# Kernel tuning notes

Measured on AMD Instinct MI355X. Metric: run time of the kernel, lower is better.

## Reference

```python
import jax, jax.numpy as jnp
import numpy as np

TEMPERATURE = 1.0
EPS = 1e-8
BATCH = 4_194_304
NUM_WEEKS = 262_144


def setup_inputs() -> dict:
    key = jax.random.key(0)
    k1, k2, k3 = jax.random.split(key, 3)
    scores = jax.random.normal(k1, (BATCH,), dtype=jnp.float32)
    labels = jax.random.normal(k2, (BATCH,), dtype=jnp.float32)
    week_indices = jnp.sort(
        jax.random.randint(k3, (BATCH,), 0, NUM_WEEKS, dtype=jnp.int32)
    )
    return {
        "scores": scores,
        "labels": labels,
        "week_indices": week_indices,
        "num_weeks": NUM_WEEKS,
    }


def _segment_softmax(x, seg, num_segments):
    # numerically stable softmax within each segment (week)
    m = jax.ops.segment_max(x, seg, num_segments=num_segments)
    e = jnp.exp(x - m[seg])
    s = jax.ops.segment_sum(e, seg, num_segments=num_segments)
    return e / s[seg]


def reference(scores, labels, week_indices, num_weeks):
    t = jnp.float32(TEMPERATURE)
    p_true = _segment_softmax(labels / t, week_indices, num_weeks)
    p_pred = _segment_softmax(scores / t, week_indices, num_weeks)
    # per-week cross-entropy: -sum p_true * log(p_pred + eps)
    per_item = p_true * jnp.log(p_pred + EPS)
    per_week = jax.ops.segment_sum(per_item, week_indices, num_segments=num_weeks)
    counts = jax.ops.segment_sum(
        jnp.ones_like(scores), week_indices, num_segments=num_weeks
    )
    valid = counts >= 2.0  # weeks with <2 items are skipped
    n_valid = jnp.sum(valid.astype(jnp.float32))
    total = -jnp.sum(jnp.where(valid, per_week, 0.0))
    return jnp.where(n_valid > 0, total / jnp.maximum(n_valid, 1.0), 0.0)
```

## Files before the change

kernel.cpp:

```cpp
#include <hip/hip_runtime.h>
#include <math.h>


#define K 16
#define TPB 256
#define CHUNK (K * TPB)
#define SLOTS 768

__device__ __forceinline__ void lds_flush(float* lel, float* les, float* ltl,
                                          int* lcnt, int s, float a, float b,
                                          float t, int c) {
    atomicAdd(&lel[s], a);
    atomicAdd(&les[s], b);
    atomicAdd(&ltl[s], t);
    atomicAdd(&lcnt[s], c);
}

__global__ __launch_bounds__(TPB) void main_pass(
        const float* __restrict__ scores, const float* __restrict__ labels,
        const int* __restrict__ widx,
        int* __restrict__ rec_week, float* __restrict__ rec_el,
        float* __restrict__ rec_es, float* __restrict__ rec_tl,
        int* __restrict__ rec_cnt,
        float* __restrict__ part_loss, int* __restrict__ part_nv) {
    __shared__ float lel[SLOTS], les[SLOTS], ltl[SLOTS];
    __shared__ int lcnt[SLOTS];
    const int tid = threadIdx.x;
    for (int s = tid; s < SLOTS; s += TPB) {
        lel[s] = 0.f; les[s] = 0.f; ltl[s] = 0.f; lcnt[s] = 0;
    }
    const int base = blockIdx.x * CHUNK;
    const int w0 = widx[base];
    const int wl = widx[base + CHUNK - 1];
    __syncthreads();

    const int t0 = base + tid * K;
    const int4   wA = *reinterpret_cast<const int4*>(widx + t0);
    const int4   wB = *reinterpret_cast<const int4*>(widx + t0 + 4);
    const int4   wC = *reinterpret_cast<const int4*>(widx + t0 + 8);
    const int4   wD = *reinterpret_cast<const int4*>(widx + t0 + 12);
    const float4 lA = *reinterpret_cast<const float4*>(labels + t0);
    const float4 lB = *reinterpret_cast<const float4*>(labels + t0 + 4);
    const float4 lC = *reinterpret_cast<const float4*>(labels + t0 + 8);
    const float4 lD = *reinterpret_cast<const float4*>(labels + t0 + 12);
    const float4 sA = *reinterpret_cast<const float4*>(scores + t0);
    const float4 sB = *reinterpret_cast<const float4*>(scores + t0 + 4);
    const float4 sC = *reinterpret_cast<const float4*>(scores + t0 + 8);
    const float4 sD = *reinterpret_cast<const float4*>(scores + t0 + 12);

    float loss = 0.f; int nv = 0;
    int cw; float ra, rb, rt; int rc;
    bool head_saved = false;
    int hs = 0; float ha = 0.f, hb = 0.f, ht = 0.f; int hc = 0;

    {
        const float el = __expf(lA.x), es = __expf(sA.x);
        cw = wA.x; ra = el; rb = es; rt = el * sA.x; rc = 1;
    }
#define ITEM(wv, lv, sv)                                                       \
    {                                                                          \
        const float el = __expf(lv), es = __expf(sv);                          \
        if ((wv) == cw) { ra += el; rb += es; rt += el * (sv); ++rc; }         \
        else {                                                                 \
            if (!head_saved) {                                                 \
                hs = cw - w0; ha = ra; hb = rb; ht = rt; hc = rc;              \
                head_saved = true;                                             \
            } else if (rc >= 2) {                                              \
                loss += rt / ra - __logf(rb); ++nv;  \
            }                                                                  \
            cw = (wv); ra = el; rb = es; rt = el * (sv); rc = 1;               \
        }                                                                      \
    }
    ITEM(wA.y, lA.y, sA.y) ITEM(wA.z, lA.z, sA.z) ITEM(wA.w, lA.w, sA.w)
    ITEM(wB.x, lB.x, sB.x) ITEM(wB.y, lB.y, sB.y) ITEM(wB.z, lB.z, sB.z) ITEM(wB.w, lB.w, sB.w)
    ITEM(wC.x, lC.x, sC.x) ITEM(wC.y, lC.y, sC.y) ITEM(wC.z, lC.z, sC.z) ITEM(wC.w, lC.w, sC.w)
    ITEM(wD.x, lD.x, sD.x) ITEM(wD.y, lD.y, sD.y) ITEM(wD.z, lD.z, sD.z) ITEM(wD.w, lD.w, sD.w)
#undef ITEM

    if (head_saved) lds_flush(lel, les, ltl, lcnt, hs, ha, hb, ht, hc);
    lds_flush(lel, les, ltl, lcnt, cw - w0, ra, rb, rt, rc);
    __syncthreads();

    const int span = wl - w0;
    for (int s = 1 + tid; s < span; s += TPB) {
        const int c = lcnt[s];
        if (c >= 2) { loss += ltl[s] / lel[s] - __logf(les[s]); ++nv; }
    }
    #pragma unroll
    for (int off = 32; off; off >>= 1) {
        loss += __shfl_down(loss, off);
        nv   += __shfl_down(nv, off);
    }
    __shared__ float ra4[4];
    __shared__ int   rn4[4];
    const int lane = tid & 63, wv4 = tid >> 6;
    if (lane == 0) { ra4[wv4] = loss; rn4[wv4] = nv; }
    __syncthreads();
    if (tid == 0) {
        part_loss[blockIdx.x] = ra4[0] + ra4[1] + ra4[2] + ra4[3];
        part_nv[blockIdx.x]   = rn4[0] + rn4[1] + rn4[2] + rn4[3];
        const int b2 = blockIdx.x * 2;
        rec_week[b2] = w0;
        rec_el[b2] = lel[0]; rec_es[b2] = les[0];
        rec_tl[b2] = ltl[0]; rec_cnt[b2] = lcnt[0];
        rec_week[b2 + 1] = wl;
        if (span > 0) {
            rec_el[b2 + 1] = lel[span]; rec_es[b2 + 1] = les[span];
            rec_tl[b2 + 1] = ltl[span]; rec_cnt[b2 + 1] = lcnt[span];
        } else {
            rec_el[b2 + 1] = 0.f; rec_es[b2 + 1] = 0.f;
            rec_tl[b2 + 1] = 0.f; rec_cnt[b2 + 1] = 0;
        }
    }
}

__global__ __launch_bounds__(1024) void finalize(
        const int* __restrict__ rec_week, const float* __restrict__ rec_el,
        const float* __restrict__ rec_es, const float* __restrict__ rec_tl,
        const int* __restrict__ rec_cnt,
        const float* __restrict__ part_loss, const int* __restrict__ part_nv,
        int nrec, int nb, float* __restrict__ out) {
    const int tid = threadIdx.x;
    float loss = 0.f; int nv = 0;
    for (int j = tid; j < nrec; j += 1024) {
        const int w = rec_week[j];
        if (j > 0 && rec_week[j - 1] == w) continue;
        float a = rec_el[j], b = rec_es[j], t = rec_tl[j];
        int c = rec_cnt[j];
        int k = j + 1;
        while (k < nrec && rec_week[k] == w) {
            a += rec_el[k]; b += rec_es[k]; t += rec_tl[k]; c += rec_cnt[k]; ++k;
        }
        if (c >= 2) { loss += t / a - __logf(b); ++nv; }
    }
    for (int j = tid; j < nb; j += 1024) { loss += part_loss[j]; nv += part_nv[j]; }
    #pragma unroll
    for (int off = 32; off; off >>= 1) {
        loss += __shfl_down(loss, off);
        nv   += __shfl_down(nv, off);
    }
    __shared__ float ra[16];
    __shared__ int   rn[16];
    const int lane = tid & 63, wv = tid >> 6;
    if (lane == 0) { ra[wv] = loss; rn[wv] = nv; }
    __syncthreads();
    if (tid == 0) {
        float tl = 0.f; int tn = 0;
        for (int k = 0; k < 16; ++k) { tl += ra[k]; tn += rn[k]; }
        out[0] = (tn > 0) ? (-tl / (float)tn) : 0.f;
    }
}

extern "C" void kernel_launch(void* const* d_in, const int* in_sizes, int n_in,
                              void* d_out, int out_size, void* d_ws, size_t ws_size,
                              hipStream_t stream) {
    const float* scores = (const float*)d_in[0];
    const float* labels = (const float*)d_in[1];
    const int*   widx   = (const int*)d_in[2];
    const int n  = in_sizes[0];
    const int nb = n / CHUNK;
    const int nrec = nb * 2;

    char* ws = (char*)d_ws;
    size_t off = 0;
    int*   rec_week = (int*)  (ws + off); off += (size_t)nrec * 4;
    float* rec_el   = (float*)(ws + off); off += (size_t)nrec * 4;
    float* rec_es   = (float*)(ws + off); off += (size_t)nrec * 4;
    float* rec_tl   = (float*)(ws + off); off += (size_t)nrec * 4;
    int*   rec_cnt  = (int*)  (ws + off); off += (size_t)nrec * 4;
    float* part_loss= (float*)(ws + off); off += (size_t)nb * 4;
    int*   part_nv  = (int*)  (ws + off);

    float* out = (float*)d_out;

    main_pass<<<nb, TPB, 0, stream>>>(scores, labels, widx,
                                      rec_week, rec_el, rec_es, rec_tl, rec_cnt,
                                      part_loss, part_nv);
    finalize<<<1, 1024, 0, stream>>>(rec_week, rec_el, rec_es, rec_tl, rec_cnt,
                                     part_loss, part_nv, nrec, nb, out);
}
```

Before: 23.22 us.

## Stage inputs through swizzled LDS with coalesced loads in two halves

Each thread no longer loads 16 contiguous elements straight from global memory. The block now loads each half of its chunk with coalesced float4 loads into swizzled shared-memory staging buffers, then each thread reads 8 contiguous elements from LDS. This aims to improve global load coalescing, since the old per-thread 64-byte strided loads were poorly coalesced. In exchange it adds extra barriers, about 24KB more LDS (which may lower occupancy), twice as many boundary flushes per thread, and shorter runs per thread, so there are more LDS atomics.

```diff
diff --git a/kernel.cpp b/kernel.cpp
--- a/kernel.cpp
+++ b/kernel.cpp
@@ -2,10 +2,13 @@
 #include <math.h>
 
 
-#define K 16
 #define TPB 256
-#define CHUNK (K * TPB)
+#define CHUNK 4096
+#define HALF 2048
+#define HF4 512
 #define SLOTS 768
+
+__device__ __forceinline__ int swz(int s) { return s ^ ((s >> 3) & 7); }
 
 __device__ __forceinline__ void lds_flush(float* lel, float* les, float* ltl,
                                           int* lcnt, int s, float a, float b,
@@ -23,6 +26,9 @@
         float* __restrict__ rec_es, float* __restrict__ rec_tl,
         int* __restrict__ rec_cnt,
         float* __restrict__ part_loss, int* __restrict__ part_nv) {
+    __shared__ int4   stg_w[HF4];
+    __shared__ float4 stg_l[HF4];
+    __shared__ float4 stg_s[HF4];
     __shared__ float lel[SLOTS], les[SLOTS], ltl[SLOTS];
     __shared__ int lcnt[SLOTS];
     const int tid = threadIdx.x;
@@ -32,31 +38,35 @@
     const int base = blockIdx.x * CHUNK;
     const int w0 = widx[base];
     const int wl = widx[base + CHUNK - 1];
-    __syncthreads();
-
-    const int t0 = base + tid * K;
-    const int4   wA = *reinterpret_cast<const int4*>(widx + t0);
-    const int4   wB = *reinterpret_cast<const int4*>(widx + t0 + 4);
-    const int4   wC = *reinterpret_cast<const int4*>(widx + t0 + 8);
-    const int4   wD = *reinterpret_cast<const int4*>(widx + t0 + 12);
-    const float4 lA = *reinterpret_cast<const float4*>(labels + t0);
-    const float4 lB = *reinterpret_cast<const float4*>(labels + t0 + 4);
-    const float4 lC = *reinterpret_cast<const float4*>(labels + t0 + 8);
-    const float4 lD = *reinterpret_cast<const float4*>(labels + t0 + 12);
-    const float4 sA = *reinterpret_cast<const float4*>(scores + t0);
-    const float4 sB = *reinterpret_cast<const float4*>(scores + t0 + 4);
-    const float4 sC = *reinterpret_cast<const float4*>(scores + t0 + 8);
-    const float4 sD = *reinterpret_cast<const float4*>(scores + t0 + 12);
 
     float loss = 0.f; int nv = 0;
-    int cw; float ra, rb, rt; int rc;
-    bool head_saved = false;
-    int hs = 0; float ha = 0.f, hb = 0.f, ht = 0.f; int hc = 0;
 
-    {
-        const float el = __expf(lA.x), es = __expf(sA.x);
-        cw = wA.x; ra = el; rb = es; rt = el * sA.x; rc = 1;
-    }
+    #pragma unroll
+    for (int h = 0; h < 2; ++h) {
+        const int hbase = base + h * HALF;
+        __syncthreads();
+        #pragma unroll
+        for (int j = 0; j < 2; ++j) {
+            const int s = j * TPB + tid;
+            const int p = swz(s);
+            stg_w[p] = *reinterpret_cast<const int4*>(widx + hbase + s * 4);
+            stg_l[p] = *reinterpret_cast<const float4*>(labels + hbase + s * 4);
+            stg_s[p] = *reinterpret_cast<const float4*>(scores + hbase + s * 4);
+        }
+        __syncthreads();
+
+        const int p0 = swz(2 * tid), p1 = swz(2 * tid + 1);
+        const int4   wA = stg_w[p0], wB = stg_w[p1];
+        const float4 lA = stg_l[p0], lB = stg_l[p1];
+        const float4 sA = stg_s[p0], sB = stg_s[p1];
+
+        int cw; float ra, rb, rt; int rc;
+        bool head_saved = false;
+        int hs = 0; float ha = 0.f, hb = 0.f, ht = 0.f; int hc = 0;
+        {
+            const float el = __expf(lA.x), es = __expf(sA.x);
+            cw = wA.x; ra = el; rb = es; rt = el * sA.x; rc = 1;
+        }
 #define ITEM(wv, lv, sv)                                                       \
     {                                                                          \
         const float el = __expf(lv), es = __expf(sv);                          \
@@ -71,14 +81,13 @@
             cw = (wv); ra = el; rb = es; rt = el * (sv); rc = 1;               \
         }                                                                      \
     }
-    ITEM(wA.y, lA.y, sA.y) ITEM(wA.z, lA.z, sA.z) ITEM(wA.w, lA.w, sA.w)
-    ITEM(wB.x, lB.x, sB.x) ITEM(wB.y, lB.y, sB.y) ITEM(wB.z, lB.z, sB.z) ITEM(wB.w, lB.w, sB.w)
-    ITEM(wC.x, lC.x, sC.x) ITEM(wC.y, lC.y, sC.y) ITEM(wC.z, lC.z, sC.z) ITEM(wC.w, lC.w, sC.w)
-    ITEM(wD.x, lD.x, sD.x) ITEM(wD.y, lD.y, sD.y) ITEM(wD.z, lD.z, sD.z) ITEM(wD.w, lD.w, sD.w)
+        ITEM(wA.y, lA.y, sA.y) ITEM(wA.z, lA.z, sA.z) ITEM(wA.w, lA.w, sA.w)
+        ITEM(wB.x, lB.x, sB.x) ITEM(wB.y, lB.y, sB.y) ITEM(wB.z, lB.z, sB.z)
+        ITEM(wB.w, lB.w, sB.w)
 #undef ITEM
-
-    if (head_saved) lds_flush(lel, les, ltl, lcnt, hs, ha, hb, ht, hc);
-    lds_flush(lel, les, ltl, lcnt, cw - w0, ra, rb, rt, rc);
+        if (head_saved) lds_flush(lel, les, ltl, lcnt, hs, ha, hb, ht, hc);
+        lds_flush(lel, les, ltl, lcnt, cw - w0, ra, rb, rt, rc);
+    }
     __syncthreads();
 
     const int span = wl - w0;
```

New measurement: 29.34 us. 1.26x slower.

## Drop LDS segment merge; emit per-thread boundary records and merge in multi-block pass

Applied to the files above, without the earlier changes.

The main pass no longer uses shared-memory atomics and block barriers to merge boundary weeks. Each thread now writes its head and tail partial week sums to global memory, and each wave writes one partial loss. A new 128-block merge kernel combines these records, and a third tiny kernel reduces the results in double precision. This removes LDS atomics and syncs from the streaming pass. In exchange it writes many more records (two per thread, about 10 MB) and adds an extra kernel launch.

```diff
diff --git a/kernel.cpp b/kernel.cpp
--- a/kernel.cpp
+++ b/kernel.cpp
@@ -2,39 +2,21 @@
 #include <math.h>
 
 
+#define TPB 256
 #define K 16
-#define TPB 256
-#define CHUNK (K * TPB)
-#define SLOTS 768
+#define CHUNK (TPB * K)
 
-__device__ __forceinline__ void lds_flush(float* lel, float* les, float* ltl,
-                                          int* lcnt, int s, float a, float b,
-                                          float t, int c) {
-    atomicAdd(&lel[s], a);
-    atomicAdd(&les[s], b);
-    atomicAdd(&ltl[s], t);
-    atomicAdd(&lcnt[s], c);
-}
-
-__global__ __launch_bounds__(TPB) void main_pass(
+__global__ __launch_bounds__(TPB) void mainpass_nolds(
         const float* __restrict__ scores, const float* __restrict__ labels,
         const int* __restrict__ widx,
         int* __restrict__ rec_week, float* __restrict__ rec_el,
         float* __restrict__ rec_es, float* __restrict__ rec_tl,
         int* __restrict__ rec_cnt,
-        float* __restrict__ part_loss, int* __restrict__ part_nv) {
-    __shared__ float lel[SLOTS], les[SLOTS], ltl[SLOTS];
-    __shared__ int lcnt[SLOTS];
+        float* __restrict__ wave_loss, int* __restrict__ wave_nv) {
     const int tid = threadIdx.x;
-    for (int s = tid; s < SLOTS; s += TPB) {
-        lel[s] = 0.f; les[s] = 0.f; ltl[s] = 0.f; lcnt[s] = 0;
-    }
-    const int base = blockIdx.x * CHUNK;
-    const int w0 = widx[base];
-    const int wl = widx[base + CHUNK - 1];
-    __syncthreads();
+    const int gtid = blockIdx.x * TPB + tid;
+    const int t0 = gtid * K;
 
-    const int t0 = base + tid * K;
     const int4   wA = *reinterpret_cast<const int4*>(widx + t0);
     const int4   wB = *reinterpret_cast<const int4*>(widx + t0 + 4);
     const int4   wC = *reinterpret_cast<const int4*>(widx + t0 + 8);
@@ -51,103 +33,113 @@
     float loss = 0.f; int nv = 0;
     int cw; float ra, rb, rt; int rc;
     bool head_saved = false;
-    int hs = 0; float ha = 0.f, hb = 0.f, ht = 0.f; int hc = 0;
-
+    int hw = 0; float ha = 0.f, hb = 0.f, ht = 0.f; int hc = 0;
     {
         const float el = __expf(lA.x), es = __expf(sA.x);
         cw = wA.x; ra = el; rb = es; rt = el * sA.x; rc = 1;
     }
-#define ITEM(wv, lv, sv)                                                       \
+#define ITEM(wv_, lv_, sv_)                                                    \
     {                                                                          \
-        const float el = __expf(lv), es = __expf(sv);                          \
-        if ((wv) == cw) { ra += el; rb += es; rt += el * (sv); ++rc; }         \
+        const float el = __expf(lv_), es = __expf(sv_);                        \
+        if ((wv_) == cw) { ra += el; rb += es; rt += el * (sv_); ++rc; }       \
         else {                                                                 \
             if (!head_saved) {                                                 \
-                hs = cw - w0; ha = ra; hb = rb; ht = rt; hc = rc;              \
+                hw = cw; ha = ra; hb = rb; ht = rt; hc = rc;                   \
                 head_saved = true;                                             \
-            } else if (rc >= 2) {                                              \
-                loss += rt / ra - __logf(rb); ++nv;  \
+            } else if (rc >= 2) {         \
+                loss += rt / ra - __logf(rb); ++nv;                            \
             }                                                                  \
-            cw = (wv); ra = el; rb = es; rt = el * (sv); rc = 1;               \
+            cw = (wv_); ra = el; rb = es; rt = el * (sv_); rc = 1;             \
         }                                                                      \
     }
     ITEM(wA.y, lA.y, sA.y) ITEM(wA.z, lA.z, sA.z) ITEM(wA.w, lA.w, sA.w)
-    ITEM(wB.x, lB.x, sB.x) ITEM(wB.y, lB.y, sB.y) ITEM(wB.z, lB.z, sB.z) ITEM(wB.w, lB.w, sB.w)
-    ITEM(wC.x, lC.x, sC.x) ITEM(wC.y, lC.y, sC.y) ITEM(wC.z, lC.z, sC.z) ITEM(wC.w, lC.w, sC.w)
-    ITEM(wD.x, lD.x, sD.x) ITEM(wD.y, lD.y, sD.y) ITEM(wD.z, lD.z, sD.z) ITEM(wD.w, lD.w, sD.w)
+    ITEM(wB.x, lB.x, sB.x) ITEM(wB.y, lB.y, sB.y) ITEM(wB.z, lB.z, sB.z)
+    ITEM(wB.w, lB.w, sB.w)
+    ITEM(wC.x, lC.x, sC.x) ITEM(wC.y, lC.y, sC.y) ITEM(wC.z, lC.z, sC.z)
+    ITEM(wC.w, lC.w, sC.w)
+    ITEM(wD.x, lD.x, sD.x) ITEM(wD.y, lD.y, sD.y) ITEM(wD.z, lD.z, sD.z)
+    ITEM(wD.w, lD.w, sD.w)
 #undef ITEM
 
-    if (head_saved) lds_flush(lel, les, ltl, lcnt, hs, ha, hb, ht, hc);
-    lds_flush(lel, les, ltl, lcnt, cw - w0, ra, rb, rt, rc);
-    __syncthreads();
+    if (!head_saved) { hw = cw; ha = 0.f; hb = 0.f; ht = 0.f; hc = 0; }
+    reinterpret_cast<int2*>(rec_week)[gtid]  = make_int2(hw, cw);
+    reinterpret_cast<float2*>(rec_el)[gtid]  = make_float2(ha, ra);
+    reinterpret_cast<float2*>(rec_es)[gtid]  = make_float2(hb, rb);
+    reinterpret_cast<float2*>(rec_tl)[gtid]  = make_float2(ht, rt);
+    reinterpret_cast<int2*>(rec_cnt)[gtid]   = make_int2(hc, rc);
 
-    const int span = wl - w0;
-    for (int s = 1 + tid; s < span; s += TPB) {
-        const int c = lcnt[s];
-        if (c >= 2) { loss += ltl[s] / lel[s] - __logf(les[s]); ++nv; }
-    }
     #pragma unroll
     for (int off = 32; off; off >>= 1) {
         loss += __shfl_down(loss, off);
         nv   += __shfl_down(nv, off);
     }
-    __shared__ float ra4[4];
-    __shared__ int   rn4[4];
-    const int lane = tid & 63, wv4 = tid >> 6;
-    if (lane == 0) { ra4[wv4] = loss; rn4[wv4] = nv; }
-    __syncthreads();
-    if (tid == 0) {
-        part_loss[blockIdx.x] = ra4[0] + ra4[1] + ra4[2] + ra4[3];
-        part_nv[blockIdx.x]   = rn4[0] + rn4[1] + rn4[2] + rn4[3];
-        const int b2 = blockIdx.x * 2;
-        rec_week[b2] = w0;
-        rec_el[b2] = lel[0]; rec_es[b2] = les[0];
-        rec_tl[b2] = ltl[0]; rec_cnt[b2] = lcnt[0];
-        rec_week[b2 + 1] = wl;
-        if (span > 0) {
-            rec_el[b2 + 1] = lel[span]; rec_es[b2 + 1] = les[span];
-            rec_tl[b2 + 1] = ltl[span]; rec_cnt[b2 + 1] = lcnt[span];
-        } else {
-            rec_el[b2 + 1] = 0.f; rec_es[b2 + 1] = 0.f;
-            rec_tl[b2 + 1] = 0.f; rec_cnt[b2 + 1] = 0;
-        }
+    if ((tid & 63) == 0) {
+        wave_loss[gtid >> 6] = loss;
+        wave_nv[gtid >> 6]   = nv;
     }
 }
 
-__global__ __launch_bounds__(1024) void finalize(
+#define MBLK 128
+
+__global__ __launch_bounds__(256) void merge_records(
         const int* __restrict__ rec_week, const float* __restrict__ rec_el,
         const float* __restrict__ rec_es, const float* __restrict__ rec_tl,
         const int* __restrict__ rec_cnt,
-        const float* __restrict__ part_loss, const int* __restrict__ part_nv,
-        int nrec, int nb, float* __restrict__ out) {
-    const int tid = threadIdx.x;
+        const float* __restrict__ wave_loss, const int* __restrict__ wave_nv,
+        int nrec, int nwave,
+        double* __restrict__ blk_loss, int* __restrict__ blk_nv) {
+    const int tid0 = blockIdx.x * blockDim.x + threadIdx.x;
+    const int stride = gridDim.x * blockDim.x;
     float loss = 0.f; int nv = 0;
-    for (int j = tid; j < nrec; j += 1024) {
+    for (int j = tid0; j < nrec; j += stride) {
         const int w = rec_week[j];
         if (j > 0 && rec_week[j - 1] == w) continue;
         float a = rec_el[j], b = rec_es[j], t = rec_tl[j];
         int c = rec_cnt[j];
-        int k = j + 1;
-        while (k < nrec && rec_week[k] == w) {
-            a += rec_el[k]; b += rec_es[k]; t += rec_tl[k]; c += rec_cnt[k]; ++k;
+        for (int k = j + 1; k < nrec && rec_week[k] == w; ++k) {
+            a += rec_el[k]; b += rec_es[k]; t += rec_tl[k]; c += rec_cnt[k];
         }
         if (c >= 2) { loss += t / a - __logf(b); ++nv; }
     }
-    for (int j = tid; j < nb; j += 1024) { loss += part_loss[j]; nv += part_nv[j]; }
+    for (int j = tid0; j < nwave; j += stride) {
+        loss += wave_loss[j]; nv += wave_nv[j];
+    }
+    double dl = (double)loss;
     #pragma unroll
     for (int off = 32; off; off >>= 1) {
-        loss += __shfl_down(loss, off);
-        nv   += __shfl_down(nv, off);
+        dl += __shfl_down(dl, off);
+        nv += __shfl_down(nv, off);
     }
-    __shared__ float ra[16];
-    __shared__ int   rn[16];
-    const int lane = tid & 63, wv = tid >> 6;
-    if (lane == 0) { ra[wv] = loss; rn[wv] = nv; }
+    __shared__ double sa[4];
+    __shared__ int    sn[4];
+    const int lane = threadIdx.x & 63, wv = threadIdx.x >> 6;
+    if (lane == 0) { sa[wv] = dl; sn[wv] = nv; }
+    __syncthreads();
+    if (threadIdx.x == 0) {
+        blk_loss[blockIdx.x] = sa[0] + sa[1] + sa[2] + sa[3];
+        blk_nv[blockIdx.x]   = sn[0] + sn[1] + sn[2] + sn[3];
+    }
+}
+
+__global__ __launch_bounds__(MBLK) void write_result(
+        const double* __restrict__ blk_loss, const int* __restrict__ blk_nv,
+        float* __restrict__ out) {
+    const int tid = threadIdx.x;
+    double dl = blk_loss[tid];
+    int    nv = blk_nv[tid];
+    #pragma unroll
+    for (int off = 32; off; off >>= 1) {
+        dl += __shfl_down(dl, off);
+        nv += __shfl_down(nv, off);
+    }
+    __shared__ double sa[2];
+    __shared__ int    sn[2];
+    if ((tid & 63) == 0) { sa[tid >> 6] = dl; sn[tid >> 6] = nv; }
     __syncthreads();
     if (tid == 0) {
-        float tl = 0.f; int tn = 0;
-        for (int k = 0; k < 16; ++k) { tl += ra[k]; tn += rn[k]; }
-        out[0] = (tn > 0) ? (-tl / (float)tn) : 0.f;
+        const double tl = sa[0] + sa[1];
+        const int    tn = sn[0] + sn[1];
+        out[0] = (tn > 0) ? (float)(-tl / (double)tn) : 0.f;
     }
 }
 
@@ -158,24 +150,30 @@
     const float* labels = (const float*)d_in[1];
     const int*   widx   = (const int*)d_in[2];
     const int n  = in_sizes[0];
-    const int nb = n / CHUNK;
-    const int nrec = nb * 2;
+    const int nthreads = n / K;
+    const int nb = nthreads / TPB;
+    const int nrec = nthreads * 2;
+    const int nwave = nthreads / 64;
 
     char* ws = (char*)d_ws;
     size_t off = 0;
-    int*   rec_week = (int*)  (ws + off); off += (size_t)nrec * 4;
-    float* rec_el   = (float*)(ws + off); off += (size_t)nrec * 4;
-    float* rec_es   = (float*)(ws + off); off += (size_t)nrec * 4;
-    float* rec_tl   = (float*)(ws + off); off += (size_t)nrec * 4;
-    int*   rec_cnt  = (int*)  (ws + off); off += (size_t)nrec * 4;
-    float* part_loss= (float*)(ws + off); off += (size_t)nb * 4;
-    int*   part_nv  = (int*)  (ws + off);
+    int*    rec_week = (int*)   (ws + off); off += (size_t)nrec * 4;
+    float*  rec_el   = (float*) (ws + off); off += (size_t)nrec * 4;
+    float*  rec_es   = (float*) (ws + off); off += (size_t)nrec * 4;
+    float*  rec_tl   = (float*) (ws + off); off += (size_t)nrec * 4;
+    int*    rec_cnt  = (int*)   (ws + off); off += (size_t)nrec * 4;
+    float*  wave_loss= (float*) (ws + off); off += (size_t)nwave * 4;
+    int*    wave_nv  = (int*)   (ws + off); off += (size_t)nwave * 4;
+    double* blk_loss = (double*)(ws + off); off += (size_t)MBLK * 8;
+    int*    blk_nv   = (int*)   (ws + off);
 
     float* out = (float*)d_out;
 
-    main_pass<<<nb, TPB, 0, stream>>>(scores, labels, widx,
-                                      rec_week, rec_el, rec_es, rec_tl, rec_cnt,
-                                      part_loss, part_nv);
-    finalize<<<1, 1024, 0, stream>>>(rec_week, rec_el, rec_es, rec_tl, rec_cnt,
-                                     part_loss, part_nv, nrec, nb, out);
+    mainpass_nolds<<<nb, TPB, 0, stream>>>(scores, labels, widx,
+                                           rec_week, rec_el, rec_es, rec_tl,
+                                           rec_cnt, wave_loss, wave_nv);
+    merge_records<<<MBLK, 256, 0, stream>>>(rec_week, rec_el, rec_es, rec_tl,
+                                            rec_cnt, wave_loss, wave_nv,
+                                            nrec, nwave, blk_loss, blk_nv);
+    write_result<<<1, MBLK, 0, stream>>>(blk_loss, blk_nv, out);
 }
```

Result: slower. 48.78 us (+110.1%).
